# Performance work log

Measured on AMD Instinct MI355X. Metric: run time of the kernel, lower is better.

Reference implementation:

```python
import jax, jax.numpy as jnp
import numpy as np

N_NODES = 50000
N_REL = 500
D_IN = 128
D_OUT = 128
D_REL = 128
NHEADS = 2
ALPHA = 0.2
E1 = 200000   # direct edges
E2 = 50000    # 2-hop paths


def _xavier(key, shape, gain=1.414):
    fan_out, fan_in = shape[-2], shape[-1]
    a = gain * np.sqrt(6.0 / (fan_in + fan_out))
    return jax.random.uniform(key, shape, jnp.float32, -a, a)


def setup_inputs() -> dict:
    key = jax.random.key(0)
    ks = jax.random.split(key, 11)
    return {
        "entity_embeddings": jax.random.normal(ks[0], (N_NODES, D_IN), jnp.float32),
        "relation_embeddings": jax.random.normal(ks[1], (N_REL, D_REL), jnp.float32),
        "entity_list": jax.random.randint(ks[2], (2, E1), 0, N_NODES),
        "relation_type": jax.random.randint(ks[3], (E1,), 0, N_REL),
        "entity_list_nhop": jax.random.randint(ks[4], (2, E2), 0, N_NODES),
        "relation_type_nhop": jax.random.randint(ks[5], (E2, 2), 0, N_REL),
        # per-head attention params: a [out, 2*in + nrela], a2 [out] (squeezed [1,out])
        "a_heads": _xavier(ks[6], (NHEADS, D_OUT, 2 * D_IN + D_REL)),
        "a2_heads": _xavier(ks[7], (NHEADS, 1, D_OUT))[:, 0, :],
        "W": _xavier(ks[8], (D_REL, NHEADS * D_OUT)),
        "a_out": _xavier(ks[9], (NHEADS * D_OUT, 3 * NHEADS * D_OUT)),
        "a2_out": _xavier(ks[10], (1, NHEADS * D_OUT))[0],
    }


def _sp_att(x, edge, eemb, a, a2, concat):
    """SpGraphAttentionLayer. x:[N,Din] edge:[2,E] eemb:[E,Drel] a:[Dout,2Din+Drel] a2:[Dout]."""
    din = x.shape[1]
    src = x[edge[0]]                       # [E, Din]
    dst = x[edge[1]]                       # [E, Din]
    # a.mm(edge_h) without materializing the [E, 2Din+Drel] concat
    edge_m = (src @ a[:, :din].T
              + dst @ a[:, din:2 * din].T
              + eemb @ a[:, 2 * din:].T)   # [E, Dout]
    edge_e = jnp.exp(-jax.nn.leaky_relu(edge_m @ a2, ALPHA))      # [E]
    rowsum = jax.ops.segment_sum(edge_e, edge[0], num_segments=x.shape[0])  # [N]
    rowsum = jnp.where(rowsum == 0.0, 1e-12, rowsum)
    h = jax.ops.segment_sum(edge_e[:, None] * edge_m, edge[0], num_segments=x.shape[0])
    h = h / rowsum[:, None]                # [N, Dout]
    return jax.nn.elu(h) if concat else h


def reference(entity_embeddings, relation_embeddings, entity_list, relation_type,
              entity_list_nhop, relation_type_nhop, a_heads, a2_heads, W, a_out, a2_out):
    ent, rel = entity_embeddings, relation_embeddings
    edge_all = jnp.concatenate([entity_list, entity_list_nhop], axis=1)   # [2, E1+E2]

    # layer-1 edge embeddings
    emb_nhop = (rel[relation_type_nhop[:, 0]] + rel[relation_type_nhop[:, 1]]
                + ent[entity_list_nhop[0]] + ent[entity_list_nhop[1]])
    edge_embed = rel[relation_type] + ent[entity_list[0]] + ent[entity_list[1]]
    eemb1 = jnp.concatenate([edge_embed, emb_nhop], axis=0)               # [E1+E2, Drel]

    # multi-head sparse attention, concat heads (torch.cat dim=1 == (N,H,D)->reshape)
    heads = jax.vmap(lambda a, a2: _sp_att(ent, edge_all, eemb1, a, a2, True))(a_heads, a2_heads)
    out1 = jnp.transpose(heads, (1, 0, 2)).reshape(ent.shape[0], -1)      # [N, H*Dout]
    # dropout p=0.0 -> identity

    out_rel = rel @ W                                                      # [R, H*Dout]
    edge_embed2 = out_rel[relation_type]
    emb_nhop2 = (out_rel[relation_type_nhop[:, 0]] + out_rel[relation_type_nhop[:, 1]]
                 + out1[entity_list_nhop[0]] + out1[entity_list_nhop[1]])
    eemb2 = jnp.concatenate([edge_embed2, emb_nhop2], axis=0)

    out_ent = jax.nn.elu(_sp_att(out1, edge_all, eemb2, a_out, a2_out, False))
    return out_ent, out_rel
```

## Files before the change

kernel.cpp:

```cpp
#include <hip/hip_runtime.h>
#include <math.h>

#define NN   50000
#define NR   500
#define E1N  200000
#define E2N  50000
#define EN   250000
#define ALPHAC 0.2f

#define OFF_OUT1  ((size_t)0)
#define OFF_EE1   ((size_t)51200000)
#define OFF_EE2   ((size_t)53200000)
#define OFF_W1    ((size_t)54200000)
#define OFF_W2    ((size_t)54203072)
#define OFF_DEG   ((size_t)54206144)
#define OFF_OFFS  ((size_t)54406144)
#define OFF_CUR   ((size_t)54606208)
#define OFF_BSUM  ((size_t)54806208)
#define OFF_CARRY ((size_t)54807232)
#define OFF_CSR   ((size_t)54808256)
#define OFF_AHH   ((size_t)55808256)
#define OFF_AHL   ((size_t)56004864)
#define OFF_AOH   ((size_t)56201472)
#define OFF_AOL   ((size_t)56594688)

typedef __attribute__((ext_vector_type(8))) short bf16x8;
typedef __attribute__((ext_vector_type(4))) short short4v;
typedef __attribute__((ext_vector_type(2))) short short2v;
typedef __attribute__((ext_vector_type(4))) float f4;
typedef __attribute__((ext_vector_type(2))) float f2;
typedef __attribute__((ext_vector_type(4))) float f32x4;

__device__ __forceinline__ float lrelu(float x) { return x > 0.f ? x : ALPHAC * x; }
__device__ __forceinline__ float eluf(float x)  { return x > 0.f ? x : expm1f(x); }

__device__ __forceinline__ short bfh(float x) {
    union { float f; unsigned u; } c; c.f = x;
    unsigned r = (c.u + 0x7FFFu + ((c.u >> 16) & 1u)) >> 16;
    return (short)r;
}
__device__ __forceinline__ float bf2f(short h) {
    union { unsigned u; float f; } c; c.u = ((unsigned)(unsigned short)h) << 16;
    return c.f;
}

__device__ __forceinline__ void decode_edge(int e, const int* el1, const int* rt1,
                                            const int* el2, const int* rtn,
                                            int& src, int& dst, int& ra, int& rb) {
    if (e < E1N) {
        src = el1[e]; dst = el1[E1N + e]; ra = rt1[e]; rb = -1;
    } else {
        int j = e - E1N;
        src = el2[j]; dst = el2[E2N + j]; ra = rtn[2 * j]; rb = rtn[2 * j + 1];
    }
}

__global__ void k_w(const float* aH, const float* a2H, const float* aO, const float* a2O,
                    float* w1, float* w2) {
    int t = blockIdx.x * blockDim.x + threadIdx.x;
    if (t < 768) {
        int h = t / 384; int r = t - h * 384; int seg = r >> 7; int j = r & 127;
        const float* A  = aH + (size_t)h * 128 * 384;
        const float* a2 = a2H + h * 128;
        float s = 0.f;
        for (int d = 0; d < 128; ++d) {
            const float* row = A + d * 384;
            float c;
            if (seg == 0)      c = row[j]       + row[256 + j];
            else if (seg == 1) c = row[128 + j] + row[256 + j];
            else               c = row[256 + j];
            s += a2[d] * c;
        }
        w1[t] = s;
    } else if (t < 1536) {
        int r = t - 768; int seg = r >> 8; int j = r & 255;
        float s = 0.f;
        for (int d = 0; d < 256; ++d) s += a2O[d] * aO[d * 768 + seg * 256 + j];
        w2[r] = s;
    }
}

__global__ void k_conv(const float* aH, const float* aO,
                       short* ahh, short* ahl, short* aoh, short* aol) {
    int t = blockIdx.x * 256 + threadIdx.x;
    if (t < 98304) {
        float x = aH[t];
        short hi = bfh(x);
        ahh[t] = hi; ahl[t] = bfh(x - bf2f(hi));
    } else if (t < 294912) {
        int i = t - 98304;
        float x = aO[i];
        short hi = bfh(x);
        aoh[i] = hi; aol[i] = bfh(x - bf2f(hi));
    }
}

__global__ void k_outrel(const float* rel, const float* W, float* outrel) {
    int r = blockIdx.x; int c = threadIdx.x;
    const float* rr = rel + r * 128;
    float s = 0.f;
    for (int k = 0; k < 128; ++k) s += rr[k] * W[k * 256 + c];
    outrel[r * 256 + c] = s;
}

__global__ void k_deg(const int* el1, const int* el2, int* deg) {
    int e = blockIdx.x * 256 + threadIdx.x;
    if (e >= EN) return;
    int src = (e < E1N) ? el1[e] : el2[e - E1N];
    atomicAdd(&deg[src], 1);
}

__global__ void k_scan1(const int* deg, int* offs, int* bsum) {
    __shared__ int s[256];
    int t = threadIdx.x; int i = blockIdx.x * 256 + t;
    int v = (i < NN) ? deg[i] : 0;
    s[t] = v; __syncthreads();
    for (int off = 1; off < 256; off <<= 1) {
        int x = (t >= off) ? s[t - off] : 0;
        __syncthreads(); s[t] += x; __syncthreads();
    }
    if (i < NN) offs[i] = s[t] - v;
    if (t == 255) bsum[blockIdx.x] = s[255];
}

__global__ void k_scan2(int* bsum, int* carry) {
    __shared__ int s[256];
    int t = threadIdx.x;
    int v = (t < 196) ? bsum[t] : 0;
    s[t] = v; __syncthreads();
    for (int off = 1; off < 256; off <<= 1) {
        int x = (t >= off) ? s[t - off] : 0;
        __syncthreads(); s[t] += x; __syncthreads();
    }
    if (t < 196) carry[t] = s[t] - v;
}

__global__ void k_scan3(int* offs, const int* carry) {
    int i = blockIdx.x * 256 + threadIdx.x;
    if (i < NN) offs[i] += carry[blockIdx.x];
}

__global__ void k_scatter(const int* el1, const int* el2, const int* offs,
                          int* cursor, int* csr) {
    int e = blockIdx.x * 256 + threadIdx.x;
    if (e >= EN) return;
    int src = (e < E1N) ? el1[e] : el2[e - E1N];
    int pos = offs[src] + atomicAdd(&cursor[src], 1);
    csr[pos] = e;
}

__global__ void k_sortcsr(const int* offs, int* csr) {
    int nid = blockIdx.x * 4 + (threadIdx.x >> 6);
    int lane = threadIdx.x & 63;
    if (nid >= NN) return;
    int start = offs[nid];
    int end = (nid == NN - 1) ? EN : offs[nid + 1];
    int len = end - start;
    if (len <= 1) return;
    if (len <= 64) {
        int key = (lane < len) ? csr[start + lane] : 0x7FFFFFFF;
        int rank = 0;
        #pragma unroll
        for (int j = 0; j < 64; ++j) {
            int kj = __shfl(key, j, 64);
            rank += (kj < key) ? 1 : 0;
        }
        if (lane < len) csr[start + rank] = key;
    } else if (lane == 0) {
        for (int i = start + 1; i < end; ++i) {
            int k = csr[i]; int j = i - 1;
            while (j >= start && csr[j] > k) { csr[j + 1] = csr[j]; --j; }
            csr[j + 1] = k;
        }
    }
}

__global__ void k_ee1(const float* ent, const float* rel,
                      const int* el1, const int* rt1, const int* el2, const int* rtn,
                      const float* w1, float* ee) {
    int wid  = (blockIdx.x * blockDim.x + threadIdx.x) >> 6;
    int lane = threadIdx.x & 63;
    int e0 = wid * 8;
    if (e0 >= EN) return;
    int d0 = lane, d1 = lane + 64;
    float wA00 = w1[d0],       wA01 = w1[d1];
    float wB00 = w1[128 + d0], wB01 = w1[128 + d1];
    float wC00 = w1[256 + d0], wC01 = w1[256 + d1];
    float wA10 = w1[384 + d0], wA11 = w1[384 + d1];
    float wB10 = w1[512 + d0], wB11 = w1[512 + d1];
    float wC10 = w1[640 + d0], wC11 = w1[640 + d1];
    int eend = min(e0 + 8, EN);
    for (int e = e0; e < eend; ++e) {
        int src, dst, ra, rb;
        decode_edge(e, el1, rt1, el2, rtn, src, dst, ra, rb);
        float es0 = ent[src * 128 + d0], es1 = ent[src * 128 + d1];
        float ed0 = ent[dst * 128 + d0], ed1 = ent[dst * 128 + d1];
        float rp0 = rel[ra * 128 + d0],  rp1 = rel[ra * 128 + d1];
        if (rb >= 0) { rp0 += rel[rb * 128 + d0]; rp1 += rel[rb * 128 + d1]; }
        float t0 = es0 * wA00 + es1 * wA01 + ed0 * wB00 + ed1 * wB01 + rp0 * wC00 + rp1 * wC01;
        float t1 = es0 * wA10 + es1 * wA11 + ed0 * wB10 + ed1 * wB11 + rp0 * wC10 + rp1 * wC11;
        #pragma unroll
        for (int off = 32; off; off >>= 1) {
            t0 += __shfl_xor(t0, off, 64);
            t1 += __shfl_xor(t1, off, 64);
        }
        if (lane == 0) {
            ee[e]      = expf(-lrelu(t0));
            ee[EN + e] = expf(-lrelu(t1));
        }
    }
}

#define PK1 392
__global__ __launch_bounds__(1024) void k_agg1(
        const float* ent, const float* rel,
        const int* el1, const int* rt1, const int* el2, const int* rtn,
        const int* offs, const int* csr, const float* ee,
        const short* ahh, const short* ahl, float* out1) {
    __shared__ __align__(16) short Yh[16 * 2 * PK1];
    __shared__ __align__(16) short Yl[16 * 2 * PK1];
    __shared__ float RS[16][2];
    int w = threadIdx.x >> 6;
    int lane = threadIdx.x & 63;
    {
        int m = w;
        int n = blockIdx.x * 16 + m;
        int start = offs[n];
        int end = (n == NN - 1) ? EN : offs[n + 1];
        f2 en = *(const f2*)&ent[n * 128 + 2 * lane];
        f2 s2a = {0, 0}, sea = {0, 0}, s2b = {0, 0}, seb = {0, 0};
        float rs0 = 0.f, rs1 = 0.f;
        for (int idx = start; idx < end; ++idx) {
            int e = csr[idx];
            int src, dst, ra, rb;
            decode_edge(e, el1, rt1, el2, rtn, src, dst, ra, rb);
            float e0v = ee[e], e1v = ee[EN + e];
            f2 gg = *(const f2*)&ent[dst * 128 + 2 * lane];
            f2 rp = *(const f2*)&rel[ra * 128 + 2 * lane];
            if (rb >= 0) rp += *(const f2*)&rel[rb * 128 + 2 * lane];
            f2 em = rp + en + gg;
            s2a += e0v * gg; sea += e0v * em;
            s2b += e1v * gg; seb += e1v * em;
            rs0 += e0v; rs1 += e1v;
        }
        f2 regs[2][3] = {{rs0 * en, s2a, sea}, {rs1 * en, s2b, seb}};
        #pragma unroll
        for (int hh = 0; hh < 2; ++hh) {
            #pragma unroll
            for (int rg = 0; rg < 3; ++rg) {
                int base = m * 2 * PK1 + hh * PK1 + rg * 128 + 2 * lane;
                short2v vh, vl;
                #pragma unroll
                for (int j = 0; j < 2; ++j) {
                    float v = regs[hh][rg][j];
                    vh[j] = bfh(v);
                    vl[j] = bfh(v - bf2f(vh[j]));
                }
                *(short2v*)&Yh[base] = vh;
                *(short2v*)&Yl[base] = vl;
            }
        }
        if (lane == 0) { RS[m][0] = rs0; RS[m][1] = rs1; }
    }
    __syncthreads();

    int r = lane & 15, g = lane >> 4;
    int ct = w;
    int h = w >> 3;
    const short* YhB = &Yh[r * 2 * PK1 + h * PK1];
    const short* YlB = &Yl[r * 2 * PK1 + h * PK1];
    const short* B0h = ahh + (size_t)(ct * 16 + r) * 384;
    const short* B0l = ahl + (size_t)(ct * 16 + r) * 384;
    f32x4 z = {0.f, 0.f, 0.f, 0.f};
    f32x4 hh0 = z, hl0 = z, lh0 = z;
    for (int kt = 0; kt < 12; ++kt) {
        int ko = kt * 32 + g * 8;
        bf16x8 yh = *(const bf16x8*)(YhB + ko);
        bf16x8 yl = *(const bf16x8*)(YlB + ko);
        bf16x8 b0h = *(const bf16x8*)(B0h + ko);
        bf16x8 b0l = *(const bf16x8*)(B0l + ko);
        hh0 = __builtin_amdgcn_mfma_f32_16x16x32_bf16(yh, b0h, hh0, 0, 0, 0);
        hl0 = __builtin_amdgcn_mfma_f32_16x16x32_bf16(yl, b0h, hl0, 0, 0, 0);
        lh0 = __builtin_amdgcn_mfma_f32_16x16x32_bf16(yh, b0l, lh0, 0, 0, 0);
    }
    f32x4 acc0 = hh0 + hl0 + lh0;
    #pragma unroll
    for (int q = 0; q < 4; ++q) {
        int m = g * 4 + q;
        float rs = RS[m][h];
        float denom = (rs == 0.f) ? 1e-12f : rs;
        size_t row = (size_t)(blockIdx.x * 16 + m) * 256;
        out1[row + ct * 16 + r] = eluf(acc0[q] / denom);
    }
}

__global__ void k_ee2(const float* out1, const float* orel,
                      const int* el1, const int* rt1, const int* el2, const int* rtn,
                      const float* w2, float* ee2) {
    int wid  = (blockIdx.x * blockDim.x + threadIdx.x) >> 6;
    int lane = threadIdx.x & 63;
    int e0 = wid * 8;
    if (e0 >= EN) return;
    f4 wS = *(const f4*)&w2[4 * lane];
    f4 wD = *(const f4*)&w2[256 + 4 * lane];
    f4 wE = *(const f4*)&w2[512 + 4 * lane];
    int eend = min(e0 + 8, EN);
    for (int e = e0; e < eend; ++e) {
        int src, dst, ra, rb;
        decode_edge(e, el1, rt1, el2, rtn, src, dst, ra, rb);
        f4 xs = *(const f4*)&out1[(size_t)src * 256 + 4 * lane];
        f4 xd = *(const f4*)&out1[(size_t)dst * 256 + 4 * lane];
        f4 em = *(const f4*)&orel[ra * 256 + 4 * lane];
        if (rb >= 0) em += *(const f4*)&orel[rb * 256 + 4 * lane] + xs + xd;
        f4 tv = xs * wS + xd * wD + em * wE;
        float t = tv[0] + tv[1] + tv[2] + tv[3];
        #pragma unroll
        for (int off = 32; off; off >>= 1) t += __shfl_xor(t, off, 64);
        if (lane == 0) ee2[e] = expf(-lrelu(t));
    }
}

#define PK2 776
__global__ __launch_bounds__(1024) void k_agg2(
        const float* out1, const float* orel,
        const int* el1, const int* rt1, const int* el2, const int* rtn,
        const int* offs, const int* csr, const float* ee2,
        const short* aoh, const short* aol, float* out_ent) {
    __shared__ __align__(16) short Yh[16 * PK2];
    __shared__ __align__(16) short Yl[16 * PK2];
    __shared__ float RS[16];
    int w = threadIdx.x >> 6;
    int lane = threadIdx.x & 63;
    {
        int m = w;
        int n = blockIdx.x * 16 + m;
        int start = offs[n];
        int end = (n == NN - 1) ? EN : offs[n + 1];
        f4 on = *(const f4*)&out1[(size_t)n * 256 + 4 * lane];
        f4 s2 = {0, 0, 0, 0}, se = {0, 0, 0, 0};
        float rs = 0.f;
        for (int idx = start; idx < end; ++idx) {
            int e = csr[idx];
            int src, dst, ra, rb;
            decode_edge(e, el1, rt1, el2, rtn, src, dst, ra, rb);
            float ev = ee2[e];
            f4 gg = *(const f4*)&out1[(size_t)dst * 256 + 4 * lane];
            f4 em = *(const f4*)&orel[ra * 256 + 4 * lane];
            if (rb >= 0) em += *(const f4*)&orel[rb * 256 + 4 * lane] + on + gg;
            s2 += ev * gg;
            se += ev * em;
            rs += ev;
        }
        f4 regs[3] = {rs * on, s2, se};
        #pragma unroll
        for (int rg = 0; rg < 3; ++rg) {
            int base = m * PK2 + rg * 256 + 4 * lane;
            short4v vh, vl;
            #pragma unroll
            for (int j = 0; j < 4; ++j) {
                float v = regs[rg][j];
                vh[j] = bfh(v);
                vl[j] = bfh(v - bf2f(vh[j]));
            }
            *(short4v*)&Yh[base] = vh;
            *(short4v*)&Yl[base] = vl;
        }
        if (lane == 0) RS[m] = rs;
    }
    __syncthreads();

    int r = lane & 15, g = lane >> 4;
    int ct = w;
    const short* YhB = &Yh[r * PK2];
    const short* YlB = &Yl[r * PK2];
    const short* B0h = aoh + (size_t)(ct * 16 + r) * 768;
    const short* B0l = aol + (size_t)(ct * 16 + r) * 768;
    f32x4 z = {0.f, 0.f, 0.f, 0.f};
    f32x4 hh0 = z, hl0 = z, lh0 = z;
    for (int kt = 0; kt < 24; ++kt) {
        int ko = kt * 32 + g * 8;
        bf16x8 yh = *(const bf16x8*)(YhB + ko);
        bf16x8 yl = *(const bf16x8*)(YlB + ko);
        bf16x8 b0h = *(const bf16x8*)(B0h + ko);
        bf16x8 b0l = *(const bf16x8*)(B0l + ko);
        hh0 = __builtin_amdgcn_mfma_f32_16x16x32_bf16(yh, b0h, hh0, 0, 0, 0);
        hl0 = __builtin_amdgcn_mfma_f32_16x16x32_bf16(yl, b0h, hl0, 0, 0, 0);
        lh0 = __builtin_amdgcn_mfma_f32_16x16x32_bf16(yh, b0l, lh0, 0, 0, 0);
    }
    f32x4 acc0 = hh0 + hl0 + lh0;
    #pragma unroll
    for (int q = 0; q < 4; ++q) {
        int m = g * 4 + q;
        float rs = RS[m];
        float denom = (rs == 0.f) ? 1e-12f : rs;
        size_t row = (size_t)(blockIdx.x * 16 + m) * 256;
        out_ent[row + ct * 16 + r] = eluf(acc0[q] / denom);
    }
}

extern "C" void kernel_launch(void* const* d_in, const int* in_sizes, int n_in,
                              void* d_out, int out_size, void* d_ws, size_t ws_size,
                              hipStream_t stream) {
    const float* ent = (const float*)d_in[0];
    const float* rel = (const float*)d_in[1];
    const int*   el1 = (const int*)d_in[2];
    const int*   rt1 = (const int*)d_in[3];
    const int*   el2 = (const int*)d_in[4];
    const int*   rtn = (const int*)d_in[5];
    const float* aH  = (const float*)d_in[6];
    const float* a2H = (const float*)d_in[7];
    const float* W   = (const float*)d_in[8];
    const float* aO  = (const float*)d_in[9];
    const float* a2O = (const float*)d_in[10];

    float* out_ent = (float*)d_out;
    float* out_rel = (float*)d_out + (size_t)NN * 256;

    char* ws = (char*)d_ws;
    float* out1   = (float*)(ws + OFF_OUT1);
    float* ee1b   = (float*)(ws + OFF_EE1);
    float* ee2b   = (float*)(ws + OFF_EE2);
    float* w1     = (float*)(ws + OFF_W1);
    float* w2     = (float*)(ws + OFF_W2);
    int*   deg    = (int*)(ws + OFF_DEG);
    int*   offs   = (int*)(ws + OFF_OFFS);
    int*   cur    = (int*)(ws + OFF_CUR);
    int*   bsum   = (int*)(ws + OFF_BSUM);
    int*   carry  = (int*)(ws + OFF_CARRY);
    int*   csr    = (int*)(ws + OFF_CSR);
    short* ahh    = (short*)(ws + OFF_AHH);
    short* ahl    = (short*)(ws + OFF_AHL);
    short* aoh    = (short*)(ws + OFF_AOH);
    short* aol    = (short*)(ws + OFF_AOL);

    hipMemsetAsync(deg, 0, (size_t)NN * 4, stream);
    hipMemsetAsync(cur, 0, (size_t)NN * 4, stream);

    k_w<<<6, 256, 0, stream>>>(aH, a2H, aO, a2O, w1, w2);
    k_conv<<<1152, 256, 0, stream>>>(aH, aO, ahh, ahl, aoh, aol);
    k_outrel<<<NR, 256, 0, stream>>>(rel, W, out_rel);

    k_deg<<<(EN + 255) / 256, 256, 0, stream>>>(el1, el2, deg);
    k_scan1<<<(NN + 255) / 256, 256, 0, stream>>>(deg, offs, bsum);
    k_scan2<<<1, 256, 0, stream>>>(bsum, carry);
    k_scan3<<<(NN + 255) / 256, 256, 0, stream>>>(offs, carry);
    k_scatter<<<(EN + 255) / 256, 256, 0, stream>>>(el1, el2, offs, cur, csr);
    k_sortcsr<<<(NN + 3) / 4, 256, 0, stream>>>(offs, csr);

    int ee_blocks = (EN / 8 + 3) / 4 + 1;
    k_ee1<<<ee_blocks, 256, 0, stream>>>(ent, rel, el1, rt1, el2, rtn, w1, ee1b);
    k_agg1<<<NN / 16, 1024, 0, stream>>>(ent, rel, el1, rt1, el2, rtn,
                                         offs, csr, ee1b, ahh, ahl, out1);
    k_ee2<<<ee_blocks, 256, 0, stream>>>(out1, out_rel, el1, rt1, el2, rtn, w2, ee2b);
    k_agg2<<<NN / 16, 1024, 0, stream>>>(out1, out_rel, el1, rt1, el2, rtn,
                                         offs, csr, ee2b, aoh, aol, out_ent);
}
```

Before: 787.9 us.

## Precompute CSR-ordered packed edge descriptors and index edge weights by CSR position

Adds a kernel that decodes each CSR-sorted edge once into a packed int4 (dst, ra, rb, src) array. The ee and agg kernels now read this descriptor contiguously and store or read edge weights in CSR order, instead of running decode_edge through scattered index loads in every kernel. This removes the repeated indirect gathers of el1/rt1/el2/rtn and the csr indirection, and makes the ee reads in the aggregation loops sequential. The cost is one extra launch and a 4 MB descriptor write and read. The ee kernels also now walk edges in CSR order, which may change gather locality for src.

```diff
diff --git a/kernel.cpp b/kernel.cpp
--- a/kernel.cpp
+++ b/kernel.cpp
@@ -23,6 +23,7 @@
 #define OFF_AHL   ((size_t)56004864)
 #define OFF_AOH   ((size_t)56201472)
 #define OFF_AOL   ((size_t)56594688)
+#define OFF_DESC  ((size_t)56987904)
 
 typedef __attribute__((ext_vector_type(8))) short bf16x8;
 typedef __attribute__((ext_vector_type(4))) short short4v;
@@ -175,13 +176,22 @@
     }
 }
 
-__global__ void k_ee1(const float* ent, const float* rel,
-                      const int* el1, const int* rt1, const int* el2, const int* rtn,
+__global__ void k_desc(const int* csr, const int* el1, const int* rt1,
+                       const int* el2, const int* rtn, int4* desc) {
+    int idx = blockIdx.x * 256 + threadIdx.x;
+    if (idx >= EN) return;
+    int e = csr[idx];
+    int src, dst, ra, rb;
+    decode_edge(e, el1, rt1, el2, rtn, src, dst, ra, rb);
+    desc[idx] = make_int4(dst, ra, rb, src);
+}
+
+__global__ void k_ee1(const float* ent, const float* rel, const int4* desc,
                       const float* w1, float* ee) {
     int wid  = (blockIdx.x * blockDim.x + threadIdx.x) >> 6;
     int lane = threadIdx.x & 63;
-    int e0 = wid * 8;
-    if (e0 >= EN) return;
+    int i0 = wid * 8;
+    if (i0 >= EN) return;
     int d0 = lane, d1 = lane + 64;
     float wA00 = w1[d0],       wA01 = w1[d1];
     float wB00 = w1[128 + d0], wB01 = w1[128 + d1];
@@ -189,10 +199,10 @@
     float wA10 = w1[384 + d0], wA11 = w1[384 + d1];
     float wB10 = w1[512 + d0], wB11 = w1[512 + d1];
     float wC10 = w1[640 + d0], wC11 = w1[640 + d1];
-    int eend = min(e0 + 8, EN);
-    for (int e = e0; e < eend; ++e) {
-        int src, dst, ra, rb;
-        decode_edge(e, el1, rt1, el2, rtn, src, dst, ra, rb);
+    int iend = min(i0 + 8, EN);
+    for (int idx = i0; idx < iend; ++idx) {
+        int4 d = desc[idx];
+        int dst = d.x, ra = d.y, rb = d.z, src = d.w;
         float es0 = ent[src * 128 + d0], es1 = ent[src * 128 + d1];
         float ed0 = ent[dst * 128 + d0], ed1 = ent[dst * 128 + d1];
         float rp0 = rel[ra * 128 + d0],  rp1 = rel[ra * 128 + d1];
@@ -205,17 +215,16 @@
             t1 += __shfl_xor(t1, off, 64);
         }
         if (lane == 0) {
-            ee[e]      = expf(-lrelu(t0));
-            ee[EN + e] = expf(-lrelu(t1));
+            ee[idx]      = expf(-lrelu(t0));
+            ee[EN + idx] = expf(-lrelu(t1));
         }
     }
 }
 
 #define PK1 392
 __global__ __launch_bounds__(1024) void k_agg1(
-        const float* ent, const float* rel,
-        const int* el1, const int* rt1, const int* el2, const int* rtn,
-        const int* offs, const int* csr, const float* ee,
+        const float* ent, const float* rel, const int4* desc,
+        const int* offs, const float* ee,
         const short* ahh, const short* ahl, float* out1) {
     __shared__ __align__(16) short Yh[16 * 2 * PK1];
     __shared__ __align__(16) short Yl[16 * 2 * PK1];
@@ -231,13 +240,11 @@
         f2 s2a = {0, 0}, sea = {0, 0}, s2b = {0, 0}, seb = {0, 0};
         float rs0 = 0.f, rs1 = 0.f;
         for (int idx = start; idx < end; ++idx) {
-            int e = csr[idx];
-            int src, dst, ra, rb;
-            decode_edge(e, el1, rt1, el2, rtn, src, dst, ra, rb);
-            float e0v = ee[e], e1v = ee[EN + e];
-            f2 gg = *(const f2*)&ent[dst * 128 + 2 * lane];
-            f2 rp = *(const f2*)&rel[ra * 128 + 2 * lane];
-            if (rb >= 0) rp += *(const f2*)&rel[rb * 128 + 2 * lane];
+            int4 d = desc[idx];
+            float e0v = ee[idx], e1v = ee[EN + idx];
+            f2 gg = *(const f2*)&ent[d.x * 128 + 2 * lane];
+            f2 rp = *(const f2*)&rel[d.y * 128 + 2 * lane];
+            if (d.z >= 0) rp += *(const f2*)&rel[d.z * 128 + 2 * lane];
             f2 em = rp + en + gg;
             s2a += e0v * gg; sea += e0v * em;
             s2b += e1v * gg; seb += e1v * em;
@@ -294,37 +301,34 @@
     }
 }
 
-__global__ void k_ee2(const float* out1, const float* orel,
-                      const int* el1, const int* rt1, const int* el2, const int* rtn,
+__global__ void k_ee2(const float* out1, const float* orel, const int4* desc,
                       const float* w2, float* ee2) {
     int wid  = (blockIdx.x * blockDim.x + threadIdx.x) >> 6;
     int lane = threadIdx.x & 63;
-    int e0 = wid * 8;
-    if (e0 >= EN) return;
+    int i0 = wid * 8;
+    if (i0 >= EN) return;
     f4 wS = *(const f4*)&w2[4 * lane];
     f4 wD = *(const f4*)&w2[256 + 4 * lane];
     f4 wE = *(const f4*)&w2[512 + 4 * lane];
-    int eend = min(e0 + 8, EN);
-    for (int e = e0; e < eend; ++e) {
-        int src, dst, ra, rb;
-        decode_edge(e, el1, rt1, el2, rtn, src, dst, ra, rb);
-        f4 xs = *(const f4*)&out1[(size_t)src * 256 + 4 * lane];
-        f4 xd = *(const f4*)&out1[(size_t)dst * 256 + 4 * lane];
-        f4 em = *(const f4*)&orel[ra * 256 + 4 * lane];
-        if (rb >= 0) em += *(const f4*)&orel[rb * 256 + 4 * lane] + xs + xd;
+    int iend = min(i0 + 8, EN);
+    for (int idx = i0; idx < iend; ++idx) {
+        int4 d = desc[idx];
+        f4 xs = *(const f4*)&out1[(size_t)d.w * 256 + 4 * lane];
+        f4 xd = *(const f4*)&out1[(size_t)d.x * 256 + 4 * lane];
+        f4 em = *(const f4*)&orel[d.y * 256 + 4 * lane];
+        if (d.z >= 0) em += *(const f4*)&orel[d.z * 256 + 4 * lane] + xs + xd;
         f4 tv = xs * wS + xd * wD + em * wE;
         float t = tv[0] + tv[1] + tv[2] + tv[3];
         #pragma unroll
         for (int off = 32; off; off >>= 1) t += __shfl_xor(t, off, 64);
-        if (lane == 0) ee2[e] = expf(-lrelu(t));
+        if (lane == 0) ee2[idx] = expf(-lrelu(t));
     }
 }
 
 #define PK2 776
 __global__ __launch_bounds__(1024) void k_agg2(
-        const float* out1, const float* orel,
-        const int* el1, const int* rt1, const int* el2, const int* rtn,
-        const int* offs, const int* csr, const float* ee2,
+        const float* out1, const float* orel, const int4* desc,
+        const int* offs, const float* ee2,
         const short* aoh, const short* aol, float* out_ent) {
     __shared__ __align__(16) short Yh[16 * PK2];
     __shared__ __align__(16) short Yl[16 * PK2];
@@ -340,13 +344,11 @@
         f4 s2 = {0, 0, 0, 0}, se = {0, 0, 0, 0};
         float rs = 0.f;
         for (int idx = start; idx < end; ++idx) {
-            int e = csr[idx];
-            int src, dst, ra, rb;
-            decode_edge(e, el1, rt1, el2, rtn, src, dst, ra, rb);
-            float ev = ee2[e];
-            f4 gg = *(const f4*)&out1[(size_t)dst * 256 + 4 * lane];
-            f4 em = *(const f4*)&orel[ra * 256 + 4 * lane];
-            if (rb >= 0) em += *(const f4*)&orel[rb * 256 + 4 * lane] + on + gg;
+            int4 d = desc[idx];
+            float ev = ee2[idx];
+            f4 gg = *(const f4*)&out1[(size_t)d.x * 256 + 4 * lane];
+            f4 em = *(const f4*)&orel[d.y * 256 + 4 * lane];
+            if (d.z >= 0) em += *(const f4*)&orel[d.z * 256 + 4 * lane] + on + gg;
             s2 += ev * gg;
             se += ev * em;
             rs += ev;
@@ -432,6 +434,7 @@
     short* ahl    = (short*)(ws + OFF_AHL);
     short* aoh    = (short*)(ws + OFF_AOH);
     short* aol    = (short*)(ws + OFF_AOL);
+    int4*  desc   = (int4*)(ws + OFF_DESC);
 
     hipMemsetAsync(deg, 0, (size_t)NN * 4, stream);
     hipMemsetAsync(cur, 0, (size_t)NN * 4, stream);
@@ -446,12 +449,13 @@
     k_scan3<<<(NN + 255) / 256, 256, 0, stream>>>(offs, carry);
     k_scatter<<<(EN + 255) / 256, 256, 0, stream>>>(el1, el2, offs, cur, csr);
     k_sortcsr<<<(NN + 3) / 4, 256, 0, stream>>>(offs, csr);
+    k_desc<<<(EN + 255) / 256, 256, 0, stream>>>(csr, el1, rt1, el2, rtn, desc);
 
     int ee_blocks = (EN / 8 + 3) / 4 + 1;
-    k_ee1<<<ee_blocks, 256, 0, stream>>>(ent, rel, el1, rt1, el2, rtn, w1, ee1b);
-    k_agg1<<<NN / 16, 1024, 0, stream>>>(ent, rel, el1, rt1, el2, rtn,
-                                         offs, csr, ee1b, ahh, ahl, out1);
-    k_ee2<<<ee_blocks, 256, 0, stream>>>(out1, out_rel, el1, rt1, el2, rtn, w2, ee2b);
-    k_agg2<<<NN / 16, 1024, 0, stream>>>(out1, out_rel, el1, rt1, el2, rtn,
-                                         offs, csr, ee2b, aoh, aol, out_ent);
-}
+    k_ee1<<<ee_blocks, 256, 0, stream>>>(ent, rel, desc, w1, ee1b);
+    k_agg1<<<NN / 16, 1024, 0, stream>>>(ent, rel, desc, offs, ee1b,
+                                         ahh, ahl, out1);
+    k_ee2<<<ee_blocks, 256, 0, stream>>>(out1, out_rel, desc, w2, ee2b);
+    k_agg2<<<NN / 16, 1024, 0, stream>>>(out1, out_rel, desc, offs, ee2b,
+                                         aoh, aol, out_ent);
+}
```

Measured after the change: 733.9 us, median of 2. -6.9%, faster.
